# Kernel tuning notes

Measured on AMD Instinct MI355X. Metric: run time of the kernel, lower is better.

## Reference

```python
import jax, jax.numpy as jnp
import numpy as np

N_NODES = 15000
N_EDGES = 60000
NODE_VOCAB = 118 + 20000
EDGE_VOCAB = 4 + 50
NODE_INDIM = 64
EDGE_INDIM = 32
H = 32          # node_hidden_feats
EH = 64         # edge_hidden_feats
NUM_STEPS = 3   # num_step_message_passing
N_BOND_TYPES = 4  # edge ids < 4 are chemical bonds -> edge_func1, else knowledge relations -> edge_func2


def setup_inputs() -> dict:
    key = jax.random.key(0)
    ks = jax.random.split(key, 20)
    s = 0.05  # param scale for numerical stability
    return {
        "node_ids": jax.random.randint(ks[0], (N_NODES,), 0, NODE_VOCAB),
        "edge_ids": jax.random.randint(ks[1], (N_EDGES,), 0, EDGE_VOCAB),
        "src": jax.random.randint(ks[2], (N_EDGES,), 0, N_NODES),
        "dst": jax.random.randint(ks[3], (N_EDGES,), 0, N_NODES),
        "node_table": jax.random.normal(ks[4], (NODE_VOCAB, NODE_INDIM), jnp.float32),
        "edge_table": jax.random.normal(ks[5], (EDGE_VOCAB, EDGE_INDIM), jnp.float32),
        "proj_W": jax.random.normal(ks[6], (H, NODE_INDIM), jnp.float32) * s,
        "proj_b": jnp.zeros((H,), jnp.float32),
        "attn_w": jax.random.normal(ks[7], (2 * H,), jnp.float32) * s,
        "e1_W1": jax.random.normal(ks[8], (EH, EDGE_INDIM), jnp.float32) * s,
        "e1_b1": jnp.zeros((EH,), jnp.float32),
        "e1_W2": jax.random.normal(ks[9], (H * H, EH), jnp.float32) * s,
        "e1_b2": jnp.zeros((H * H,), jnp.float32),
        "e2_W1": jax.random.normal(ks[10], (EH, EDGE_INDIM), jnp.float32) * s,
        "e2_b1": jnp.zeros((EH,), jnp.float32),
        "e2_W2": jax.random.normal(ks[11], (H * H, EH), jnp.float32) * s,
        "e2_b2": jnp.zeros((H * H,), jnp.float32),
        "gru_Wih": jax.random.normal(ks[12], (3 * H, H), jnp.float32) * s,
        "gru_Whh": jax.random.normal(ks[13], (3 * H, H), jnp.float32) * s,
        "gru_bih": jnp.zeros((3 * H,), jnp.float32),
        "gru_bhh": jnp.zeros((3 * H,), jnp.float32),
    }


def _edge_softmax(logits, dst, num_nodes):
    # softmax over incoming edges of each destination node
    m = jax.ops.segment_max(logits, dst, num_segments=num_nodes)
    ex = jnp.exp(logits - m[dst])
    s = jax.ops.segment_sum(ex, dst, num_segments=num_nodes)
    return ex / s[dst]


def reference(node_ids, edge_ids, src, dst, node_table, edge_table, proj_W, proj_b,
              attn_w, e1_W1, e1_b1, e1_W2, e1_b2, e2_W1, e2_b1, e2_W2, e2_b2,
              gru_Wih, gru_Whh, gru_bih, gru_bhh):
    # --- embedding lookups ---
    nf = node_table[node_ids]                      # [N, node_indim]
    ef = edge_table[edge_ids]                      # [E, edge_indim]
    # --- project node feats: Linear + ReLU ---
    h = jax.nn.relu(nf @ proj_W.T + proj_b)        # [N, H]

    # --- per-edge weight matrices from the two edge MLPs (edge feats are
    # constant across message-passing steps, so compute once) ---
    def edge_mlp(W1, b1, W2, b2):
        z = jax.nn.relu(ef @ W1.T + b1)            # [E, EH]
        return (z @ W2.T + b2).reshape(-1, H, H)   # [E, H, H]

    W_e1 = edge_mlp(e1_W1, e1_b1, e1_W2, e1_b2)
    W_e2 = edge_mlp(e2_W1, e2_b1, e2_W2, e2_b2)
    is_bond = (edge_ids < N_BOND_TYPES)[:, None, None]
    W_edge = jnp.where(is_bond, W_e1, W_e2)        # [E, H, H]

    hidden = h                                     # GRU hidden state (seq of len 1 -> GRUCell)
    for _ in range(NUM_STEPS):
        # attention logits on edges: leaky_relu(attn_fc([h_src || h_dst]))
        a = jax.nn.leaky_relu(
            h[src] @ attn_w[:H] + h[dst] @ attn_w[H:])     # [E]
        alpha = _edge_softmax(a, dst, N_NODES)             # [E]
        # edge-conditioned message: (h_src @ W_e) weighted by attention
        msg = jnp.einsum('ei,eio->eo', h[src], W_edge) * alpha[:, None]  # [E, H]
        agg = jax.ops.segment_sum(msg, dst, num_segments=N_NODES)       # [N, H]
        m = jax.nn.relu(agg)
        # single GRU step (torch nn.GRU, 1 layer, seq_len 1)
        gi = m @ gru_Wih.T + gru_bih               # [N, 3H]
        gh = hidden @ gru_Whh.T + gru_bhh          # [N, 3H]
        ir, iz, inn = jnp.split(gi, 3, axis=1)
        hr, hz, hn = jnp.split(gh, 3, axis=1)
        r = jax.nn.sigmoid(ir + hr)
        z = jax.nn.sigmoid(iz + hz)
        n = jnp.tanh(inn + r * hn)
        hidden = (1.0 - z) * n + z * hidden
        h = hidden
    return h
```

## Files before the change

### kernel.cpp

```cpp
#include <hip/hip_runtime.h>
#include <hip/hip_bf16.h>
#include <math.h>

#define N_NODES   15000
#define N_EDGES   60000
#define EVOCAB    54
#define NODE_INDIM 64
#define EDGE_INDIM 32
#define H  32
#define EH 64
#define N_BOND 4

#define TASK_VOCAB (EVOCAB * 1024)
#define TASK_PROJ  (N_NODES * H)
#define TASK_ZERO  ((N_NODES * H + N_NODES) / 4)
#define TASK_PACK  (3 * H * H)
#define TA (TASK_VOCAB + TASK_PROJ + TASK_ZERO + TASK_PACK)

__global__ void setup_kernel(const int* __restrict__ node_ids,
                             const float* __restrict__ node_table,
                             const float* __restrict__ edge_table,
                             const float* __restrict__ proj_W, const float* __restrict__ proj_b,
                             const float* __restrict__ e1_W1, const float* __restrict__ e1_b1,
                             const float* __restrict__ e1_W2, const float* __restrict__ e1_b2,
                             const float* __restrict__ e2_W1, const float* __restrict__ e2_b1,
                             const float* __restrict__ e2_W2, const float* __restrict__ e2_b2,
                             const float* __restrict__ gWih, const float* __restrict__ gWhh,
                             float* __restrict__ Wt, float* __restrict__ h,
                             float* __restrict__ agg,
                             float4* __restrict__ Wpk4, float2* __restrict__ Wpk2) {
    int t = blockIdx.x * 256 + threadIdx.x;
    if (t >= TA) return;
    if (t < TASK_VOCAB) {
        int v = t >> 10, f = t & 1023, l = t & 63;
        const float* W1 = (v < N_BOND) ? e1_W1 : e2_W1;
        const float* b1 = (v < N_BOND) ? e1_b1 : e2_b1;
        const float* W2 = (v < N_BOND) ? e1_W2 : e2_W2;
        const float* b2 = (v < N_BOND) ? e1_b2 : e2_b2;
        const float* ef = edge_table + v * EDGE_INDIM;
        float z = b1[l];
        const float* w1r = W1 + l * EDGE_INDIM;
        #pragma unroll
        for (int j = 0; j < EDGE_INDIM; ++j) z += ef[j] * w1r[j];
        z = fmaxf(z, 0.f);
        float y = b2[f];
        const float* w2r = W2 + f * EH;
        #pragma unroll
        for (int k = 0; k < EH; ++k) y += __shfl(z, k, 64) * w2r[k];
        Wt[v * 1024 + f] = y;
    } else if (t < TASK_VOCAB + TASK_PROJ) {
        int q = t - TASK_VOCAB;
        int n = q >> 5, o = q & 31;
        int gid = node_ids[n];
        const float* nf = node_table + (size_t)gid * NODE_INDIM;
        const float* wr = proj_W + o * NODE_INDIM;
        float acc = proj_b[o];
        #pragma unroll 8
        for (int j = 0; j < NODE_INDIM; ++j) acc += nf[j] * wr[j];
        h[q] = fmaxf(acc, 0.f);
    } else if (t < TASK_VOCAB + TASK_PROJ + TASK_ZERO) {
        int q = t - TASK_VOCAB - TASK_PROJ;
        ((float4*)agg)[q] = make_float4(0.f, 0.f, 0.f, 0.f);
    } else {
        int q = t - TASK_VOCAB - TASK_PROJ - TASK_ZERO;
        int j = q >> 5, o = q & 31;
        Wpk4[q] = make_float4(gWih[o * 32 + j], gWih[(32 + o) * 32 + j],
                              gWih[(64 + o) * 32 + j], gWhh[o * 32 + j]);
        Wpk2[q] = make_float2(gWhh[(32 + o) * 32 + j], gWhh[(64 + o) * 32 + j]);
    }
}

__launch_bounds__(256)
__global__ void edge_kernel(const int* __restrict__ src, const int* __restrict__ dst,
                            const int* __restrict__ edge_ids,
                            const float* __restrict__ h, const float* __restrict__ Wt,
                            const float* __restrict__ attn_w,
                            float* __restrict__ agg, float* __restrict__ sm) {
    int t = blockIdx.x * 256 + threadIdx.x;
    int e = t >> 5, o = t & 31;
    int s = src[e], d = dst[e], v = edge_ids[e];
    float hs = h[s * 32 + o];
    float val = hs * attn_w[o] + h[d * 32 + o] * attn_w[32 + o];
    #pragma unroll
    for (int k = 16; k > 0; k >>= 1) val += __shfl_xor(val, k, 32);
    float a  = (val > 0.f) ? val : 0.01f * val;
    float ex = __expf(a);
    const float* W = Wt + v * 1024 + o;
    float y = 0.f;
    #pragma unroll
    for (int i = 0; i < 32; ++i)
        y += __shfl(hs, i, 32) * W[i * 32];
    atomicAdd(&agg[d * 32 + o], ex * y);
    if (o == 0) atomicAdd(&sm[d], ex);
}

__launch_bounds__(256)
__global__ void gru_kernel(float* __restrict__ agg, float* __restrict__ sm,
                           const float* __restrict__ h,
                           const float4* __restrict__ Wpk4, const float2* __restrict__ Wpk2,
                           const float* __restrict__ gbih, const float* __restrict__ gbhh,
                           float* __restrict__ hout) {
    int t = blockIdx.x * 256 + threadIdx.x;
    int n = t >> 5, o = t & 31;
    float sinv = 1.f / sm[n];
    float m  = fmaxf(agg[t] * sinv, 0.f);
    float hv = h[t];
    float gir = 0.f, giz = 0.f, gin = 0.f, ghr = 0.f, ghz = 0.f, ghn = 0.f;
    #pragma unroll 8
    for (int j = 0; j < 32; ++j) {
        float mj = __shfl(m, j, 32);
        float hj = __shfl(hv, j, 32);
        float4 a = Wpk4[j * 32 + o];
        float2 b = Wpk2[j * 32 + o];
        gir += mj * a.x;  giz += mj * a.y;  gin += mj * a.z;
        ghr += hj * a.w;  ghz += hj * b.x;  ghn += hj * b.y;
    }
    float r  = 1.f / (1.f + __expf(-(gir + gbih[o]      + ghr + gbhh[o])));
    float z  = 1.f / (1.f + __expf(-(giz + gbih[32 + o] + ghz + gbhh[32 + o])));
    float nn = tanhf(gin + gbih[64 + o] + r * (ghn + gbhh[64 + o]));
    hout[t] = (1.f - z) * nn + z * hv;
    agg[t] = 0.f;
    if (o == 0) sm[n] = 0.f;
}

extern "C" void kernel_launch(void* const* d_in, const int* in_sizes, int n_in,
                              void* d_out, int out_size, void* d_ws, size_t ws_size,
                              hipStream_t stream) {
    const int*   node_ids   = (const int*)d_in[0];
    const int*   edge_ids   = (const int*)d_in[1];
    const int*   src        = (const int*)d_in[2];
    const int*   dst        = (const int*)d_in[3];
    const float* node_table = (const float*)d_in[4];
    const float* edge_table = (const float*)d_in[5];
    const float* proj_W     = (const float*)d_in[6];
    const float* proj_b     = (const float*)d_in[7];
    const float* attn_w     = (const float*)d_in[8];
    const float* e1_W1 = (const float*)d_in[9];  const float* e1_b1 = (const float*)d_in[10];
    const float* e1_W2 = (const float*)d_in[11]; const float* e1_b2 = (const float*)d_in[12];
    const float* e2_W1 = (const float*)d_in[13]; const float* e2_b1 = (const float*)d_in[14];
    const float* e2_W2 = (const float*)d_in[15]; const float* e2_b2 = (const float*)d_in[16];
    const float* gWih  = (const float*)d_in[17]; const float* gWhh  = (const float*)d_in[18];
    const float* gbih  = (const float*)d_in[19]; const float* gbhh  = (const float*)d_in[20];

    char* ws = (char*)d_ws;
    float*  Wt   = (float*)(ws);
    float*  h    = (float*)(ws + 221184);
    float*  agg  = (float*)(ws + 221184 + 1920000);
    float*  sm   = (float*)(ws + 221184 + 3840000);
    float4* Wpk4 = (float4*)(ws + 221184 + 3840000 + 60000);
    float2* Wpk2 = (float2*)(ws + 221184 + 3840000 + 60000 + 49152);
    float*  out  = (float*)d_out;

    setup_kernel<<<(TA + 255) / 256, 256, 0, stream>>>(
        node_ids, node_table, edge_table, proj_W, proj_b,
        e1_W1, e1_b1, e1_W2, e1_b2, e2_W1, e2_b1, e2_W2, e2_b2,
        gWih, gWhh, Wt, h, agg, Wpk4, Wpk2);

    for (int step = 0; step < 3; ++step) {
        edge_kernel<<<(N_EDGES * 32) / 256, 256, 0, stream>>>(
            src, dst, edge_ids, h, Wt, attn_w, agg, sm);
        float* hout = (step == 2) ? out : h;
        gru_kernel<<<(N_NODES * 32) / 256, 256, 0, stream>>>(
            agg, sm, h, Wpk4, Wpk2, gbih, gbhh, hout);
    }
}
```

Measured before the change: 225.9 us.

## Fuse pipeline into cooperative kernel with dst-sorted CSR pull aggregation

Replaces the setup, edge and GRU launches with one cooperative persistent kernel that uses grid-wide syncs between phases. Each call builds a CSR grouping of edges by destination (count, prefix scan in one block, scatter of packed src/edge-id). Each node then pulls its incoming edges and computes attention, messages, softmax normalisation and the GRU update in one pass, with no float atomics and no zeroing of accumulators. The trade-off is per-call CSR construction, several grid barriers, a serial scan in a single block, and per-node loops that diverge with node degree. A fallback to the old multi-kernel path is kept in case the cooperative launch fails.

```diff
diff --git a/kernel.cpp b/kernel.cpp
--- a/kernel.cpp
+++ b/kernel.cpp
@@ -1,6 +1,8 @@
 #include <hip/hip_runtime.h>
-#include <hip/hip_bf16.h>
+#include <hip/hip_cooperative_groups.h>
 #include <math.h>
+
+namespace cg = cooperative_groups;
 
 #define N_NODES   15000
 #define N_EDGES   60000
@@ -13,9 +15,161 @@
 
 #define TASK_VOCAB (EVOCAB * 1024)
 #define TASK_PROJ  (N_NODES * H)
-#define TASK_ZERO  ((N_NODES * H + N_NODES) / 4)
-#define TASK_PACK  (3 * H * H)
-#define TA (TASK_VOCAB + TASK_PROJ + TASK_ZERO + TASK_PACK)
+#define TASK_PACK  (H * H)
+#define PH0_TOTAL  (TASK_VOCAB + TASK_PROJ + TASK_PACK + N_NODES)
+
+__global__ __launch_bounds__(256)
+void fused_kernel(const int* __restrict__ node_ids, const int* __restrict__ edge_ids,
+                  const int* __restrict__ src, const int* __restrict__ dst,
+                  const float* __restrict__ node_table, const float* __restrict__ edge_table,
+                  const float* __restrict__ proj_W, const float* __restrict__ proj_b,
+                  const float* __restrict__ attn_w,
+                  const float* __restrict__ e1_W1, const float* __restrict__ e1_b1,
+                  const float* __restrict__ e1_W2, const float* __restrict__ e1_b2,
+                  const float* __restrict__ e2_W1, const float* __restrict__ e2_b1,
+                  const float* __restrict__ e2_W2, const float* __restrict__ e2_b2,
+                  const float* __restrict__ gWih, const float* __restrict__ gWhh,
+                  const float* __restrict__ gbih, const float* __restrict__ gbhh,
+                  float* __restrict__ Wt, float* __restrict__ h0, float* __restrict__ h1,
+                  int* __restrict__ rs, int* __restrict__ edge_p,
+                  float4* __restrict__ Wpk4, float2* __restrict__ Wpk2,
+                  float* __restrict__ out)
+{
+    cg::grid_group grid = cg::this_grid();
+    const int T  = gridDim.x * 256;
+    const int t0 = blockIdx.x * 256 + threadIdx.x;
+
+    for (int t = t0; t < PH0_TOTAL; t += T) {
+        if (t < TASK_VOCAB) {
+            int v = t >> 10, f = t & 1023, l = t & 63;
+            const float* W1 = (v < N_BOND) ? e1_W1 : e2_W1;
+            const float* b1 = (v < N_BOND) ? e1_b1 : e2_b1;
+            const float* W2 = (v < N_BOND) ? e1_W2 : e2_W2;
+            const float* b2 = (v < N_BOND) ? e1_b2 : e2_b2;
+            const float* ef = edge_table + v * EDGE_INDIM;
+            float z = b1[l];
+            const float* w1r = W1 + l * EDGE_INDIM;
+            #pragma unroll
+            for (int j = 0; j < EDGE_INDIM; ++j) z += ef[j] * w1r[j];
+            z = fmaxf(z, 0.f);
+            float y = b2[f];
+            const float* w2r = W2 + f * EH;
+            #pragma unroll
+            for (int k = 0; k < EH; ++k) y += __shfl(z, k, 64) * w2r[k];
+            Wt[(v << 10) + f] = y;
+        } else if (t < TASK_VOCAB + TASK_PROJ) {
+            int q = t - TASK_VOCAB;
+            int n = q >> 5, o = q & 31;
+            int gid = node_ids[n];
+            const float* nf = node_table + (size_t)gid * NODE_INDIM;
+            const float* wr = proj_W + o * NODE_INDIM;
+            float acc = proj_b[o];
+            #pragma unroll 8
+            for (int j = 0; j < NODE_INDIM; ++j) acc += nf[j] * wr[j];
+            h0[q] = fmaxf(acc, 0.f);
+        } else if (t < TASK_VOCAB + TASK_PROJ + TASK_PACK) {
+            int q = t - (TASK_VOCAB + TASK_PROJ);
+            int j = q >> 5, o = q & 31;
+            Wpk4[q] = make_float4(gWih[o * 32 + j], gWih[(32 + o) * 32 + j],
+                                  gWih[(64 + o) * 32 + j], gWhh[o * 32 + j]);
+            Wpk2[q] = make_float2(gWhh[(32 + o) * 32 + j], gWhh[(64 + o) * 32 + j]);
+        } else {
+            rs[t - (TASK_VOCAB + TASK_PROJ + TASK_PACK)] = 0;
+        }
+    }
+    grid.sync();
+
+    for (int e = t0; e < N_EDGES; e += T) atomicAdd(&rs[dst[e]], 1);
+    grid.sync();
+
+    if (blockIdx.x == 0) {
+        __shared__ int s_sum[256];
+        __shared__ int s_wsum[4];
+        const int CH = (N_NODES + 255) / 256;
+        int base = threadIdx.x * CH;
+        int sum = 0;
+        for (int k = 0; k < CH; ++k) { int i = base + k; if (i < N_NODES) sum += rs[i]; }
+        s_sum[threadIdx.x] = sum;
+        __syncthreads();
+        int lane = threadIdx.x & 63, wv = threadIdx.x >> 6;
+        int v = s_sum[threadIdx.x];
+        #pragma unroll
+        for (int off = 1; off < 64; off <<= 1) {
+            int u = __shfl_up(v, off, 64);
+            if (lane >= off) v += u;
+        }
+        if (lane == 63) s_wsum[wv] = v;
+        __syncthreads();
+        int wbase = 0;
+        for (int w = 0; w < wv; ++w) wbase += s_wsum[w];
+        int run = wbase + (v - sum);
+        for (int k = 0; k < CH; ++k) {
+            int i = base + k;
+            if (i < N_NODES) { int d = rs[i]; rs[i] = run; run += d; }
+        }
+    }
+    grid.sync();
+
+    for (int e = t0; e < N_EDGES; e += T) {
+        int pos = atomicAdd(&rs[dst[e]], 1);
+        edge_p[pos] = src[e] | (edge_ids[e] << 16);
+    }
+    grid.sync();
+
+    float* hc = h0;
+    float* hn = h1;
+    for (int step = 0; step < 3; ++step) {
+        float* op = (step == 2) ? out : hn;
+        for (int t = t0; t < N_NODES * H; t += T) {
+            int n = t >> 5, o = t & 31;
+            int pbeg = (n == 0) ? 0 : rs[n - 1];
+            int pend = rs[n];
+            float hv = hc[t];
+            float w1 = attn_w[o], w2 = attn_w[32 + o];
+            float bd = hv * w2;
+            #pragma unroll
+            for (int k = 16; k > 0; k >>= 1) bd += __shfl_xor(bd, k, 32);
+            float sex = 0.f, acc = 0.f;
+            for (int p = pbeg; p < pend; ++p) {
+                int pk = edge_p[p];
+                int sp = pk & 0xFFFF, vp = pk >> 16;
+                float hs = hc[(sp << 5) + o];
+                float as = hs * w1;
+                #pragma unroll
+                for (int k = 16; k > 0; k >>= 1) as += __shfl_xor(as, k, 32);
+                float a = as + bd;
+                a = (a > 0.f) ? a : 0.01f * a;
+                float ex = __expf(a);
+                sex += ex;
+                const float* W = Wt + (vp << 10) + o;
+                float y = 0.f;
+                #pragma unroll
+                for (int i = 0; i < 32; ++i) y += __shfl(hs, i, 32) * W[i * 32];
+                acc += ex * y;
+            }
+            float m = (pend > pbeg) ? fmaxf(acc / sex, 0.f) : 0.f;
+            float gir = 0.f, giz = 0.f, gin = 0.f, ghr = 0.f, ghz = 0.f, ghn = 0.f;
+            #pragma unroll 4
+            for (int j = 0; j < 32; ++j) {
+                float mj = __shfl(m, j, 32);
+                float hj = __shfl(hv, j, 32);
+                float4 a4 = Wpk4[j * 32 + o];
+                float2 b2 = Wpk2[j * 32 + o];
+                gir += mj * a4.x;  giz += mj * a4.y;  gin += mj * a4.z;
+                ghr += hj * a4.w;  ghz += hj * b2.x;  ghn += hj * b2.y;
+            }
+            float r  = 1.f / (1.f + __expf(-(gir + gbih[o]      + ghr + gbhh[o])));
+            float z  = 1.f / (1.f + __expf(-(giz + gbih[32 + o] + ghz + gbhh[32 + o])));
+            float nn = tanhf(gin + gbih[64 + o] + r * (ghn + gbhh[64 + o]));
+            op[t] = (1.f - z) * nn + z * hv;
+        }
+        if (step < 2) grid.sync();
+        float* tmp = hc; hc = hn; hn = tmp;
+    }
+}
+
+#define FB_TASK_ZERO ((N_NODES * H + N_NODES) / 4)
+#define FB_TA (TASK_VOCAB + TASK_PROJ + FB_TASK_ZERO + TASK_PACK)
 
 __global__ void setup_kernel(const int* __restrict__ node_ids,
                              const float* __restrict__ node_table,
@@ -30,7 +184,7 @@
                              float* __restrict__ agg,
                              float4* __restrict__ Wpk4, float2* __restrict__ Wpk2) {
     int t = blockIdx.x * 256 + threadIdx.x;
-    if (t >= TA) return;
+    if (t >= FB_TA) return;
     if (t < TASK_VOCAB) {
         int v = t >> 10, f = t & 1023, l = t & 63;
         const float* W1 = (v < N_BOND) ? e1_W1 : e2_W1;
@@ -58,11 +212,11 @@
         #pragma unroll 8
         for (int j = 0; j < NODE_INDIM; ++j) acc += nf[j] * wr[j];
         h[q] = fmaxf(acc, 0.f);
-    } else if (t < TASK_VOCAB + TASK_PROJ + TASK_ZERO) {
+    } else if (t < TASK_VOCAB + TASK_PROJ + FB_TASK_ZERO) {
         int q = t - TASK_VOCAB - TASK_PROJ;
         ((float4*)agg)[q] = make_float4(0.f, 0.f, 0.f, 0.f);
     } else {
-        int q = t - TASK_VOCAB - TASK_PROJ - TASK_ZERO;
+        int q = t - TASK_VOCAB - TASK_PROJ - FB_TASK_ZERO;
         int j = q >> 5, o = q & 31;
         Wpk4[q] = make_float4(gWih[o * 32 + j], gWih[(32 + o) * 32 + j],
                               gWih[(64 + o) * 32 + j], gWhh[o * 32 + j]);
@@ -128,8 +282,8 @@
                               hipStream_t stream) {
     const int*   node_ids   = (const int*)d_in[0];
     const int*   edge_ids   = (const int*)d_in[1];
-    const int*   src        = (const int*)d_in[2];
-    const int*   dst        = (const int*)d_in[3];
+    const int*   srcp       = (const int*)d_in[2];
+    const int*   dstp       = (const int*)d_in[3];
     const float* node_table = (const float*)d_in[4];
     const float* edge_table = (const float*)d_in[5];
     const float* proj_W     = (const float*)d_in[6];
@@ -141,26 +295,64 @@
     const float* e2_W2 = (const float*)d_in[15]; const float* e2_b2 = (const float*)d_in[16];
     const float* gWih  = (const float*)d_in[17]; const float* gWhh  = (const float*)d_in[18];
     const float* gbih  = (const float*)d_in[19]; const float* gbhh  = (const float*)d_in[20];
+    float* outp = (float*)d_out;
 
     char* ws = (char*)d_ws;
     float*  Wt   = (float*)(ws);
-    float*  h    = (float*)(ws + 221184);
-    float*  agg  = (float*)(ws + 221184 + 1920000);
-    float*  sm   = (float*)(ws + 221184 + 3840000);
-    float4* Wpk4 = (float4*)(ws + 221184 + 3840000 + 60000);
-    float2* Wpk2 = (float2*)(ws + 221184 + 3840000 + 60000 + 49152);
-    float*  out  = (float*)d_out;
-
-    setup_kernel<<<(TA + 255) / 256, 256, 0, stream>>>(
-        node_ids, node_table, edge_table, proj_W, proj_b,
-        e1_W1, e1_b1, e1_W2, e1_b2, e2_W1, e2_b1, e2_W2, e2_b2,
-        gWih, gWhh, Wt, h, agg, Wpk4, Wpk2);
-
-    for (int step = 0; step < 3; ++step) {
-        edge_kernel<<<(N_EDGES * 32) / 256, 256, 0, stream>>>(
-            src, dst, edge_ids, h, Wt, attn_w, agg, sm);
-        float* hout = (step == 2) ? out : h;
-        gru_kernel<<<(N_NODES * 32) / 256, 256, 0, stream>>>(
-            agg, sm, h, Wpk4, Wpk2, gbih, gbhh, hout);
-    }
-}
+    float*  h0b  = (float*)(ws + 221184);
+    float*  h1b  = (float*)(ws + 2141184);
+    int*    rs   = (int*)  (ws + 4061184);
+    int*    ep   = (int*)  (ws + 4121184);
+    float4* Wpk4 = (float4*)(ws + 4361184);
+    float2* Wpk2 = (float2*)(ws + 4377568);
+
+    static int coop_grid = -2;
+    if (coop_grid == -2) {
+        int nb = 0;
+        hipError_t qe = hipOccupancyMaxActiveBlocksPerMultiprocessor(&nb, fused_kernel, 256, 0);
+        if (qe == hipSuccess && nb > 0) {
+            long g = (long)nb * 256;
+            if (g > 2048) g = 2048;
+            coop_grid = (int)g;
+        } else {
+            coop_grid = -1;
+        }
+        (void)hipGetLastError();
+    }
+
+    hipError_t lerr = hipErrorUnknown;
+    if (coop_grid > 0) {
+        void* args[] = {
+            (void*)&node_ids, (void*)&edge_ids, (void*)&srcp, (void*)&dstp,
+            (void*)&node_table, (void*)&edge_table, (void*)&proj_W, (void*)&proj_b,
+            (void*)&attn_w,
+            (void*)&e1_W1, (void*)&e1_b1, (void*)&e1_W2, (void*)&e1_b2,
+            (void*)&e2_W1, (void*)&e2_b1, (void*)&e2_W2, (void*)&e2_b2,
+            (void*)&gWih, (void*)&gWhh, (void*)&gbih, (void*)&gbhh,
+            (void*)&Wt, (void*)&h0b, (void*)&h1b, (void*)&rs, (void*)&ep,
+            (void*)&Wpk4, (void*)&Wpk2, (void*)&outp
+        };
+        lerr = hipLaunchCooperativeKernel(fused_kernel, dim3(coop_grid), dim3(256),
+                                          args, 0, stream);
+        if (lerr != hipSuccess) { (void)hipGetLastError(); coop_grid = -1; }
+    }
+
+    if (lerr != hipSuccess) {
+        float*  h    = (float*)(ws + 221184);
+        float*  agg  = (float*)(ws + 2141184);
+        float*  sm   = (float*)(ws + 4061184);
+        float4* fW4  = (float4*)(ws + 4121184);
+        float2* fW2  = (float2*)(ws + 4137568);
+        setup_kernel<<<(FB_TA + 255) / 256, 256, 0, stream>>>(
+            node_ids, node_table, edge_table, proj_W, proj_b,
+            e1_W1, e1_b1, e1_W2, e1_b2, e2_W1, e2_b1, e2_W2, e2_b2,
+            gWih, gWhh, Wt, h, agg, fW4, fW2);
+        for (int step = 0; step < 3; ++step) {
+            edge_kernel<<<(N_EDGES * 32) / 256, 256, 0, stream>>>(
+                srcp, dstp, edge_ids, h, Wt, attn_w, agg, sm);
+            float* hout = (step == 2) ? outp : h;
+            gru_kernel<<<(N_NODES * 32) / 256, 256, 0, stream>>>(
+                agg, sm, h, fW4, fW2, gbih, gbhh, hout);
+        }
+    }
+}
```

Measured after the change: 554.2 us. 145% more time.

## Replace atomic edge scatter with CSR-by-destination gather fused with GRU

Applied to the files above, without the earlier changes.

Builds a CSR grouping of edges by destination (degree count, single-block scan, scatter of packed src/edge-type), then fuses message aggregation and the GRU update into one per-node kernel that walks its incoming edges. This removes the per-step float atomics into agg/sm and their zeroing, and precomputes the per-node attention dot products so the edge loop needs only two scalar loads. It adds setup kernels, a serial-ish single-block scan, and per-node load imbalance from varying in-degree. Vectorized float4 loads are also used in setup.

```diff
diff --git a/kernel.cpp b/kernel.cpp
--- a/kernel.cpp
+++ b/kernel.cpp
@@ -1,5 +1,4 @@
 #include <hip/hip_runtime.h>
-#include <hip/hip_bf16.h>
 #include <math.h>
 
 #define N_NODES   15000
@@ -13,114 +12,196 @@
 
 #define TASK_VOCAB (EVOCAB * 1024)
 #define TASK_PROJ  (N_NODES * H)
-#define TASK_ZERO  ((N_NODES * H + N_NODES) / 4)
-#define TASK_PACK  (3 * H * H)
-#define TA (TASK_VOCAB + TASK_PROJ + TASK_ZERO + TASK_PACK)
-
-__global__ void setup_kernel(const int* __restrict__ node_ids,
-                             const float* __restrict__ node_table,
-                             const float* __restrict__ edge_table,
-                             const float* __restrict__ proj_W, const float* __restrict__ proj_b,
-                             const float* __restrict__ e1_W1, const float* __restrict__ e1_b1,
-                             const float* __restrict__ e1_W2, const float* __restrict__ e1_b2,
-                             const float* __restrict__ e2_W1, const float* __restrict__ e2_b1,
-                             const float* __restrict__ e2_W2, const float* __restrict__ e2_b2,
-                             const float* __restrict__ gWih, const float* __restrict__ gWhh,
-                             float* __restrict__ Wt, float* __restrict__ h,
-                             float* __restrict__ agg,
-                             float4* __restrict__ Wpk4, float2* __restrict__ Wpk2) {
+#define TASK_PACK  (H * H)
+#define TASK_DEG_BASE (TASK_VOCAB + TASK_PROJ + TASK_PACK)
+#define TA_TOTAL   (TASK_DEG_BASE + N_EDGES)
+
+#define WT_OFF  0
+#define H0_OFF  221184
+#define H1_OFF  2141184
+#define EPK_OFF 4061184
+#define W4_OFF  4301184
+#define W2_OFF  4317568
+#define RS_OFF  4325760
+#define LS0_OFF 4385760
+#define BS0_OFF 4445760
+#define LS1_OFF 4505760
+#define BS1_OFF 4565760
+
+__global__ __launch_bounds__(256)
+void setup_kernel(const int* __restrict__ node_ids, const int* __restrict__ dst,
+                  const float* __restrict__ node_table, const float* __restrict__ edge_table,
+                  const float* __restrict__ proj_W, const float* __restrict__ proj_b,
+                  const float* __restrict__ attn_w,
+                  const float* __restrict__ e1_W1, const float* __restrict__ e1_b1,
+                  const float* __restrict__ e1_W2, const float* __restrict__ e1_b2,
+                  const float* __restrict__ e2_W1, const float* __restrict__ e2_b1,
+                  const float* __restrict__ e2_W2, const float* __restrict__ e2_b2,
+                  const float* __restrict__ gWih, const float* __restrict__ gWhh,
+                  float* __restrict__ Wt, float* __restrict__ h0,
+                  float* __restrict__ ls, float* __restrict__ bs,
+                  float4* __restrict__ Wpk4, float2* __restrict__ Wpk2,
+                  int* __restrict__ rs)
+{
     int t = blockIdx.x * 256 + threadIdx.x;
-    if (t >= TA) return;
+    if (t >= TA_TOTAL) return;
     if (t < TASK_VOCAB) {
         int v = t >> 10, f = t & 1023, l = t & 63;
         const float* W1 = (v < N_BOND) ? e1_W1 : e2_W1;
         const float* b1 = (v < N_BOND) ? e1_b1 : e2_b1;
         const float* W2 = (v < N_BOND) ? e1_W2 : e2_W2;
         const float* b2 = (v < N_BOND) ? e1_b2 : e2_b2;
-        const float* ef = edge_table + v * EDGE_INDIM;
+        const float4* ef4 = (const float4*)(edge_table + v * EDGE_INDIM);
+        const float4* w14 = (const float4*)(W1 + l * EDGE_INDIM);
         float z = b1[l];
-        const float* w1r = W1 + l * EDGE_INDIM;
-        #pragma unroll
-        for (int j = 0; j < EDGE_INDIM; ++j) z += ef[j] * w1r[j];
+        #pragma unroll
+        for (int j = 0; j < 8; ++j) {
+            float4 a = ef4[j], b = w14[j];
+            z += a.x*b.x + a.y*b.y + a.z*b.z + a.w*b.w;
+        }
         z = fmaxf(z, 0.f);
         float y = b2[f];
-        const float* w2r = W2 + f * EH;
-        #pragma unroll
-        for (int k = 0; k < EH; ++k) y += __shfl(z, k, 64) * w2r[k];
-        Wt[v * 1024 + f] = y;
+        const float4* w24 = (const float4*)(W2 + f * EH);
+        #pragma unroll
+        for (int k = 0; k < 16; ++k) {
+            float4 w = w24[k];
+            y += __shfl(z, 4*k,   64) * w.x + __shfl(z, 4*k+1, 64) * w.y
+               + __shfl(z, 4*k+2, 64) * w.z + __shfl(z, 4*k+3, 64) * w.w;
+        }
+        Wt[(v << 10) + f] = y;
     } else if (t < TASK_VOCAB + TASK_PROJ) {
         int q = t - TASK_VOCAB;
         int n = q >> 5, o = q & 31;
         int gid = node_ids[n];
-        const float* nf = node_table + (size_t)gid * NODE_INDIM;
-        const float* wr = proj_W + o * NODE_INDIM;
+        const float4* nf4 = (const float4*)(node_table + (size_t)gid * NODE_INDIM);
+        const float4* wr4 = (const float4*)(proj_W + o * NODE_INDIM);
         float acc = proj_b[o];
-        #pragma unroll 8
-        for (int j = 0; j < NODE_INDIM; ++j) acc += nf[j] * wr[j];
-        h[q] = fmaxf(acc, 0.f);
-    } else if (t < TASK_VOCAB + TASK_PROJ + TASK_ZERO) {
-        int q = t - TASK_VOCAB - TASK_PROJ;
-        ((float4*)agg)[q] = make_float4(0.f, 0.f, 0.f, 0.f);
-    } else {
-        int q = t - TASK_VOCAB - TASK_PROJ - TASK_ZERO;
+        #pragma unroll
+        for (int j = 0; j < 16; ++j) {
+            float4 a = nf4[j], b = wr4[j];
+            acc += a.x*b.x + a.y*b.y + a.z*b.z + a.w*b.w;
+        }
+        float hval = fmaxf(acc, 0.f);
+        h0[q] = hval;
+        float c1 = hval * attn_w[o], c2 = hval * attn_w[32 + o];
+        #pragma unroll
+        for (int k = 16; k > 0; k >>= 1) {
+            c1 += __shfl_xor(c1, k, 32);
+            c2 += __shfl_xor(c2, k, 32);
+        }
+        if (o == 0) { ls[n] = c1; bs[n] = c2; }
+    } else if (t < TASK_DEG_BASE) {
+        int q = t - (TASK_VOCAB + TASK_PROJ);
         int j = q >> 5, o = q & 31;
         Wpk4[q] = make_float4(gWih[o * 32 + j], gWih[(32 + o) * 32 + j],
                               gWih[(64 + o) * 32 + j], gWhh[o * 32 + j]);
         Wpk2[q] = make_float2(gWhh[(32 + o) * 32 + j], gWhh[(64 + o) * 32 + j]);
-    }
-}
-
-__launch_bounds__(256)
-__global__ void edge_kernel(const int* __restrict__ src, const int* __restrict__ dst,
-                            const int* __restrict__ edge_ids,
-                            const float* __restrict__ h, const float* __restrict__ Wt,
-                            const float* __restrict__ attn_w,
-                            float* __restrict__ agg, float* __restrict__ sm) {
-    int t = blockIdx.x * 256 + threadIdx.x;
-    int e = t >> 5, o = t & 31;
-    int s = src[e], d = dst[e], v = edge_ids[e];
-    float hs = h[s * 32 + o];
-    float val = hs * attn_w[o] + h[d * 32 + o] * attn_w[32 + o];
+    } else {
+        atomicAdd(&rs[dst[t - TASK_DEG_BASE]], 1);
+    }
+}
+
+__global__ __launch_bounds__(256)
+void scan_kernel(int* __restrict__ rs)
+{
+    __shared__ int s_sum[256];
+    __shared__ int s_wsum[4];
+    const int CH = (N_NODES + 255) / 256;
+    int base = threadIdx.x * CH;
+    int sum = 0;
+    for (int k = 0; k < CH; ++k) { int i = base + k; if (i < N_NODES) sum += rs[i]; }
+    s_sum[threadIdx.x] = sum;
+    __syncthreads();
+    int lane = threadIdx.x & 63, wv = threadIdx.x >> 6;
+    int v = s_sum[threadIdx.x];
     #pragma unroll
-    for (int k = 16; k > 0; k >>= 1) val += __shfl_xor(val, k, 32);
-    float a  = (val > 0.f) ? val : 0.01f * val;
-    float ex = __expf(a);
-    const float* W = Wt + v * 1024 + o;
-    float y = 0.f;
-    #pragma unroll
-    for (int i = 0; i < 32; ++i)
-        y += __shfl(hs, i, 32) * W[i * 32];
-    atomicAdd(&agg[d * 32 + o], ex * y);
-    if (o == 0) atomicAdd(&sm[d], ex);
-}
-
-__launch_bounds__(256)
-__global__ void gru_kernel(float* __restrict__ agg, float* __restrict__ sm,
-                           const float* __restrict__ h,
-                           const float4* __restrict__ Wpk4, const float2* __restrict__ Wpk2,
-                           const float* __restrict__ gbih, const float* __restrict__ gbhh,
-                           float* __restrict__ hout) {
+    for (int off = 1; off < 64; off <<= 1) {
+        int u = __shfl_up(v, off, 64);
+        if (lane >= off) v += u;
+    }
+    if (lane == 63) s_wsum[wv] = v;
+    __syncthreads();
+    int wbase = 0;
+    for (int w = 0; w < wv; ++w) wbase += s_wsum[w];
+    int run = wbase + (v - sum);
+    for (int k = 0; k < CH; ++k) {
+        int i = base + k;
+        if (i < N_NODES) { int d = rs[i]; rs[i] = run; run += d; }
+    }
+}
+
+__global__ __launch_bounds__(256)
+void scatter_kernel(const int* __restrict__ src, const int* __restrict__ dst,
+                    const int* __restrict__ eid,
+                    int* __restrict__ rs, int* __restrict__ edge_p)
+{
+    int e = blockIdx.x * 256 + threadIdx.x;
+    if (e >= N_EDGES) return;
+    int pos = atomicAdd(&rs[dst[e]], 1);
+    edge_p[pos] = src[e] | (eid[e] << 16);
+}
+
+__global__ __launch_bounds__(256)
+void mp_kernel(const int* __restrict__ rs, const int* __restrict__ edge_p,
+               const float* __restrict__ hc, const float* __restrict__ Wt,
+               const float* __restrict__ attn_w,
+               const float4* __restrict__ Wpk4, const float2* __restrict__ Wpk2,
+               const float* __restrict__ gbih, const float* __restrict__ gbhh,
+               const float* __restrict__ lsc, const float* __restrict__ bsc,
+               float* __restrict__ lsn, float* __restrict__ bsn,
+               float* __restrict__ op, int last)
+{
     int t = blockIdx.x * 256 + threadIdx.x;
     int n = t >> 5, o = t & 31;
-    float sinv = 1.f / sm[n];
-    float m  = fmaxf(agg[t] * sinv, 0.f);
-    float hv = h[t];
+    int pbeg = (n == 0) ? 0 : rs[n - 1];
+    int pend = rs[n];
+    float hv = hc[t];
+    float bdn = bsc[n];
+    float sex = 0.f, acc = 0.f;
+    for (int p = pbeg; p < pend; ++p) {
+        int pk = edge_p[p];
+        int sp = pk & 0xFFFF, vp = pk >> 16;
+        float a = lsc[sp] + bdn;
+        a = (a > 0.f) ? a : 0.01f * a;
+        float ex = __expf(a);
+        sex += ex;
+        float hs = hc[(sp << 5) + o];
+        const float* W = Wt + (vp << 10) + o;
+        float y0 = 0.f, y1 = 0.f, y2 = 0.f, y3 = 0.f;
+        #pragma unroll
+        for (int i = 0; i < 8; ++i) {
+            y0 += __shfl(hs, 4*i,     32) * W[(4*i    ) * 32];
+            y1 += __shfl(hs, 4*i + 1, 32) * W[(4*i + 1) * 32];
+            y2 += __shfl(hs, 4*i + 2, 32) * W[(4*i + 2) * 32];
+            y3 += __shfl(hs, 4*i + 3, 32) * W[(4*i + 3) * 32];
+        }
+        acc += ex * ((y0 + y1) + (y2 + y3));
+    }
+    float m = (pend > pbeg) ? fmaxf(acc / sex, 0.f) : 0.f;
     float gir = 0.f, giz = 0.f, gin = 0.f, ghr = 0.f, ghz = 0.f, ghn = 0.f;
-    #pragma unroll 8
+    #pragma unroll 4
     for (int j = 0; j < 32; ++j) {
         float mj = __shfl(m, j, 32);
         float hj = __shfl(hv, j, 32);
-        float4 a = Wpk4[j * 32 + o];
-        float2 b = Wpk2[j * 32 + o];
-        gir += mj * a.x;  giz += mj * a.y;  gin += mj * a.z;
-        ghr += hj * a.w;  ghz += hj * b.x;  ghn += hj * b.y;
+        float4 a4 = Wpk4[j * 32 + o];
+        float2 b2 = Wpk2[j * 32 + o];
+        gir += mj * a4.x;  giz += mj * a4.y;  gin += mj * a4.z;
+        ghr += hj * a4.w;  ghz += hj * b2.x;  ghn += hj * b2.y;
     }
     float r  = 1.f / (1.f + __expf(-(gir + gbih[o]      + ghr + gbhh[o])));
     float z  = 1.f / (1.f + __expf(-(giz + gbih[32 + o] + ghz + gbhh[32 + o])));
     float nn = tanhf(gin + gbih[64 + o] + r * (ghn + gbhh[64 + o]));
-    hout[t] = (1.f - z) * nn + z * hv;
-    agg[t] = 0.f;
-    if (o == 0) sm[n] = 0.f;
+    float hid = (1.f - z) * nn + z * hv;
+    op[t] = hid;
+    if (!last) {
+        float c1 = hid * attn_w[o], c2 = hid * attn_w[32 + o];
+        #pragma unroll
+        for (int k = 16; k > 0; k >>= 1) {
+            c1 += __shfl_xor(c1, k, 32);
+            c2 += __shfl_xor(c2, k, 32);
+        }
+        if (o == 0) { lsn[n] = c1; bsn[n] = c2; }
+    }
 }
 
 extern "C" void kernel_launch(void* const* d_in, const int* in_sizes, int n_in,
@@ -128,8 +209,8 @@
                               hipStream_t stream) {
     const int*   node_ids   = (const int*)d_in[0];
     const int*   edge_ids   = (const int*)d_in[1];
-    const int*   src        = (const int*)d_in[2];
-    const int*   dst        = (const int*)d_in[3];
+    const int*   srcp       = (const int*)d_in[2];
+    const int*   dstp       = (const int*)d_in[3];
     const float* node_table = (const float*)d_in[4];
     const float* edge_table = (const float*)d_in[5];
     const float* proj_W     = (const float*)d_in[6];
@@ -141,26 +222,45 @@
     const float* e2_W2 = (const float*)d_in[15]; const float* e2_b2 = (const float*)d_in[16];
     const float* gWih  = (const float*)d_in[17]; const float* gWhh  = (const float*)d_in[18];
     const float* gbih  = (const float*)d_in[19]; const float* gbhh  = (const float*)d_in[20];
+    float* outp = (float*)d_out;
 
     char* ws = (char*)d_ws;
-    float*  Wt   = (float*)(ws);
-    float*  h    = (float*)(ws + 221184);
-    float*  agg  = (float*)(ws + 221184 + 1920000);
-    float*  sm   = (float*)(ws + 221184 + 3840000);
-    float4* Wpk4 = (float4*)(ws + 221184 + 3840000 + 60000);
-    float2* Wpk2 = (float2*)(ws + 221184 + 3840000 + 60000 + 49152);
-    float*  out  = (float*)d_out;
-
-    setup_kernel<<<(TA + 255) / 256, 256, 0, stream>>>(
-        node_ids, node_table, edge_table, proj_W, proj_b,
+    float*  Wt   = (float*)(ws + WT_OFF);
+    float*  h0b  = (float*)(ws + H0_OFF);
+    float*  h1b  = (float*)(ws + H1_OFF);
+    int*    epk  = (int*)  (ws + EPK_OFF);
+    float4* Wpk4 = (float4*)(ws + W4_OFF);
+    float2* Wpk2 = (float2*)(ws + W2_OFF);
+    int*    rs   = (int*)  (ws + RS_OFF);
+    float*  ls0  = (float*)(ws + LS0_OFF);
+    float*  bs0  = (float*)(ws + BS0_OFF);
+    float*  ls1  = (float*)(ws + LS1_OFF);
+    float*  bs1  = (float*)(ws + BS1_OFF);
+
+    hipMemsetAsync(ws + RS_OFF, 0, 60000, stream);
+
+    setup_kernel<<<(TA_TOTAL + 255) / 256, 256, 0, stream>>>(
+        node_ids, dstp, node_table, edge_table, proj_W, proj_b, attn_w,
         e1_W1, e1_b1, e1_W2, e1_b2, e2_W1, e2_b1, e2_W2, e2_b2,
-        gWih, gWhh, Wt, h, agg, Wpk4, Wpk2);
-
+        gWih, gWhh, Wt, h0b, ls0, bs0, Wpk4, Wpk2, rs);
+
+    scan_kernel<<<1, 256, 0, stream>>>(rs);
+
+    scatter_kernel<<<(N_EDGES + 255) / 256, 256, 0, stream>>>(
+        srcp, dstp, edge_ids, rs, epk);
+
+    float* hc = h0b;  float* hn = h1b;
+    float* lc = ls0;  float* bc = bs0;
+    float* ln = ls1;  float* bn = bs1;
     for (int step = 0; step < 3; ++step) {
-        edge_kernel<<<(N_EDGES * 32) / 256, 256, 0, stream>>>(
-            src, dst, edge_ids, h, Wt, attn_w, agg, sm);
-        float* hout = (step == 2) ? out : h;
-        gru_kernel<<<(N_NODES * 32) / 256, 256, 0, stream>>>(
-            agg, sm, h, Wpk4, Wpk2, gbih, gbhh, hout);
-    }
-}
+        int last = (step == 2);
+        float* op = last ? outp : hn;
+        mp_kernel<<<(N_NODES * H) / 256, 256, 0, stream>>>(
+            rs, epk, hc, Wt, attn_w, Wpk4, Wpk2, gbih, gbhh,
+            lc, bc, ln, bn, op, last);
+        float* tf;
+        tf = hc; hc = hn; hn = tf;
+        tf = lc; lc = ln; ln = tf;
+        tf = bc; bc = bn; bn = tf;
+    }
+}
```

New measurement: 294.4 us. 1.3x slower.
